# Performance work log

Measured on AMD Instinct MI355X. Metric: run time of the kernel, lower is better.

## Reference

```python
import jax, jax.numpy as jnp
import numpy as np

# bitsandbytes NF4 codebook (16 levels)
NF4_CODE = jnp.array([
    -1.0, -0.6961928009986877, -0.5250730514526367, -0.39491748809814453,
    -0.28444138169288635, -0.18477343022823334, -0.09105003625154495, 0.0,
    0.07958029955625534, 0.16093020141124725, 0.24611230194568634,
    0.33791524171829224, 0.44070982933044434, 0.5626170039176941,
    0.7229568362236023, 1.0], dtype=jnp.float32)

L, D, KV, F, V = 2, 4096, 1024, 14336, 32000   # layers, d_model, kv_dim, ffn, vocab
H, HK, HD = 32, 8, 128                          # q heads, kv heads, head dim
B, S = 2, 1024
BLK = 64                                        # NF4 quant blocksize
ROPE_THETA = 500000.0
RMS_EPS = 1e-5


def _dequant(idx, absmax, shape):
    # idx: uint8 flat codes in [0,16); absmax: fp32 per-64-element block scale
    w = NF4_CODE[idx.astype(jnp.int32)]
    return (w.reshape(-1, BLK) * absmax[:, None]).reshape(shape)


def _rmsnorm(x, w):
    return x * jax.lax.rsqrt(jnp.mean(x * x, axis=-1, keepdims=True) + RMS_EPS) * w


def _rope(x, cos, sin):
    d2 = x.shape[-1] // 2
    x1, x2 = x[..., :d2], x[..., d2:]
    return jnp.concatenate([x1 * cos - x2 * sin, x2 * cos + x1 * sin], axis=-1)


def setup_inputs() -> dict:
    key = jax.random.key(0)
    ks = iter(jax.random.split(key, 64))

    def idx(n):
        return jax.random.randint(next(ks), (n,), 0, 16).astype(jnp.uint8)

    def amax(n):
        return jax.random.uniform(next(ks), (n // BLK,), minval=0.01, maxval=0.05)

    def qw(n):
        return (jnp.stack([idx(n) for _ in range(L)]),
                jnp.stack([amax(n) for _ in range(L)]))

    inp = {}
    inp["input_ids"] = jax.random.randint(next(ks), (B, S), 0, V, dtype=jnp.int32)
    inp["attention_mask"] = jnp.ones((B, S), dtype=jnp.int32)
    inp["embed"] = jax.random.normal(next(ks), (V, D), dtype=jnp.float32) * 0.02
    inp["q_idx"], inp["q_absmax"] = qw(D * D)
    inp["k_idx"], inp["k_absmax"] = qw(KV * D)
    inp["v_idx"], inp["v_absmax"] = qw(KV * D)
    inp["o_idx"], inp["o_absmax"] = qw(D * D)
    inp["gate_idx"], inp["gate_absmax"] = qw(F * D)
    inp["up_idx"], inp["up_absmax"] = qw(F * D)
    inp["down_idx"], inp["down_absmax"] = qw(D * F)
    inp["ln1_w"] = jnp.ones((L, D), dtype=jnp.float32)
    inp["ln2_w"] = jnp.ones((L, D), dtype=jnp.float32)
    inp["final_ln_w"] = jnp.ones((D,), dtype=jnp.float32)
    return inp


def reference(input_ids, attention_mask, embed,
              q_idx, q_absmax, k_idx, k_absmax, v_idx, v_absmax,
              o_idx, o_absmax, gate_idx, gate_absmax, up_idx, up_absmax,
              down_idx, down_absmax, ln1_w, ln2_w, final_ln_w):
    b, s = input_ids.shape
    h = embed[input_ids]                                  # [B,S,D]
    pos = jnp.arange(s, dtype=jnp.float32)
    inv = 1.0 / (ROPE_THETA ** (jnp.arange(0, HD, 2, dtype=jnp.float32) / HD))
    ang = pos[:, None] * inv[None, :]                     # [S,HD/2]
    cos = jnp.cos(ang)[None, :, None, :]
    sin = jnp.sin(ang)[None, :, None, :]
    causal = jnp.tril(jnp.ones((s, s), dtype=bool))
    mask = causal[None, None] & (attention_mask[:, None, None, :] > 0)  # [B,1,S,S]
    neg = jnp.finfo(h.dtype).min

    for l in range(L):
        x = _rmsnorm(h, ln1_w[l])
        q = x @ _dequant(q_idx[l], q_absmax[l], (D, D)).T
        k = x @ _dequant(k_idx[l], k_absmax[l], (KV, D)).T
        v = x @ _dequant(v_idx[l], v_absmax[l], (KV, D)).T
        q = _rope(q.reshape(b, s, H, HD), cos, sin)
        k = _rope(k.reshape(b, s, HK, HD), cos, sin)
        v = v.reshape(b, s, HK, HD)
        k = jnp.repeat(k, H // HK, axis=2)                # GQA expand
        v = jnp.repeat(v, H // HK, axis=2)
        scores = jnp.einsum('bqhd,bkhd->bhqk', q, k) / np.float32(np.sqrt(HD))
        scores = jnp.where(mask, scores, neg)
        attn = jax.nn.softmax(scores, axis=-1)
        ctx = jnp.einsum('bhqk,bkhd->bqhd', attn, v).reshape(b, s, D)
        h = h + ctx @ _dequant(o_idx[l], o_absmax[l], (D, D)).T
        x = _rmsnorm(h, ln2_w[l])
        g = x @ _dequant(gate_idx[l], gate_absmax[l], (F, D)).T
        u = x @ _dequant(up_idx[l], up_absmax[l], (F, D)).T
        h = h + (jax.nn.silu(g) * u) @ _dequant(down_idx[l], down_absmax[l], (D, F)).T

    h = _rmsnorm(h, final_ln_w)                           # last hidden state
    m = attention_mask.astype(h.dtype)[..., None]         # masked mean pool
    pooled = (h * m).sum(axis=1) / jnp.clip(m.sum(axis=1), 1e-9)
    return pooled
```

## Files before the change

### kernel.cpp

```cpp
#include <hip/hip_runtime.h>
#include <hip/hip_fp16.h>
#include <cstdint>
#include <cstddef>

#define B_  2
#define S_  1024
#define D_  4096
#define KV_ 1024
#define F_  14336
#define H_  32
#define HK_ 8
#define HD_ 128
#define M_  2048

typedef _Float16 f16;
typedef f16   f16x8 __attribute__((ext_vector_type(8)));
typedef f16   f16x4 __attribute__((ext_vector_type(4)));
typedef float f32x4 __attribute__((ext_vector_type(4)));

#define AS1(p) ((const __attribute__((address_space(1))) void*)(p))
#define AS3(p) ((__attribute__((address_space(3))) void*)(p))

__device__ __constant__ float NF4_C[16] = {
 -1.0f, -0.6961928009986877f, -0.5250730514526367f, -0.39491748809814453f,
 -0.28444138169288635f, -0.18477343022823334f, -0.09105003625154495f, 0.0f,
 0.07958029955625534f, 0.16093020141124725f, 0.24611230194568634f,
 0.33791524171829224f, 0.44070982933044434f, 0.5626170039176941f,
 0.7229568362236023f, 1.0f };

__global__ void k_detect(const unsigned* __restrict__ p, int* __restrict__ flag){
    if (threadIdx.x == 0){
        int u8 = 0;
        for (int i = 0; i < 256; ++i) if (p[i] >= 16u) { u8 = 1; break; }
        *flag = u8;
    }
}

__global__ __launch_bounds__(256) void k_dequant(const void* __restrict__ idxBase, size_t elemOff,
        const float* __restrict__ amax, f16* __restrict__ out, const int* __restrict__ flag)
{
    __shared__ __half2 T[3856];
    int t = threadIdx.x;
    if (t < 256){
        int b0 = t & 15, b1 = t >> 4;
        T[b0 + (b1 << 8)] = __halves2half2(__float2half(NF4_C[b0]), __float2half(NF4_C[b1]));
    }
    __syncthreads();
    size_t i = ((size_t)blockIdx.x * 256 + t) * 16;
    float am = amax[i >> 6];
    __half2 am2 = __float2half2_rn(am);
    union { __half2 h2[8]; uint4 u4[2]; } R;
    if (*flag){
        uint4 u = *(const uint4*)((const uint8_t*)idxBase + elemOff + i);
        unsigned w[4] = {u.x, u.y, u.z, u.w};
        #pragma unroll
        for (int j = 0; j < 4; ++j){
            R.h2[j*2+0] = __hmul2(T[w[j] & 0xFFFFu], am2);
            R.h2[j*2+1] = __hmul2(T[w[j] >> 16],     am2);
        }
    } else {
        const int4* s4 = (const int4*)((const int*)idxBase + elemOff + i);
        #pragma unroll
        for (int j = 0; j < 4; ++j){
            int4 a = s4[j];
            R.h2[j*2+0] = __hmul2(T[a.x | (a.y << 8)], am2);
            R.h2[j*2+1] = __hmul2(T[a.z | (a.w << 8)], am2);
        }
    }
    uint4* o = (uint4*)(out + i);
    o[0] = R.u4[0]; o[1] = R.u4[1];
}

__global__ __launch_bounds__(256) void k_dequant3(const void* __restrict__ qi, const void* __restrict__ ki,
        const void* __restrict__ vi, const float* __restrict__ qa, const float* __restrict__ ka,
        const float* __restrict__ va, size_t oDD, size_t oKVD, f16* __restrict__ out,
        const int* __restrict__ flag)
{
    __shared__ __half2 T[3856];
    int t = threadIdx.x;
    if (t < 256){
        int b0 = t & 15, b1 = t >> 4;
        T[b0 + (b1 << 8)] = __halves2half2(__float2half(NF4_C[b0]), __float2half(NF4_C[b1]));
    }
    __syncthreads();
    int blk = blockIdx.x;
    const void* src; const float* am; size_t so; f16* dst;
    const size_t DDc = (size_t)D_ * D_, KVDc = (size_t)KV_ * D_;
    if (blk < 4096)      { src = qi; am = qa; so = oDD;  dst = out; }
    else if (blk < 5120) { src = ki; am = ka; so = oKVD; dst = out + DDc;        blk -= 4096; }
    else                 { src = vi; am = va; so = oKVD; dst = out + DDc + KVDc; blk -= 5120; }
    size_t i = ((size_t)blk * 256 + t) * 16;
    float amv = am[(so + i) >> 6];
    __half2 am2 = __float2half2_rn(amv);
    union { __half2 h2[8]; uint4 u4[2]; } R;
    if (*flag){
        uint4 u = *(const uint4*)((const uint8_t*)src + so + i);
        unsigned w[4] = {u.x, u.y, u.z, u.w};
        #pragma unroll
        for (int j = 0; j < 4; ++j){
            R.h2[j*2+0] = __hmul2(T[w[j] & 0xFFFFu], am2);
            R.h2[j*2+1] = __hmul2(T[w[j] >> 16],     am2);
        }
    } else {
        const int4* s4 = (const int4*)((const int*)src + so + i);
        #pragma unroll
        for (int j = 0; j < 4; ++j){
            int4 a = s4[j];
            R.h2[j*2+0] = __hmul2(T[a.x | (a.y << 8)], am2);
            R.h2[j*2+1] = __hmul2(T[a.z | (a.w << 8)], am2);
        }
    }
    uint4* o = (uint4*)(dst + i);
    o[0] = R.u4[0]; o[1] = R.u4[1];
}

__global__ __launch_bounds__(256) void k_embed(const int* __restrict__ ids,
        const float* __restrict__ E, float* __restrict__ Hh)
{
    int row = blockIdx.x, t = threadIdx.x;
    int id = ids[row];
    const float4* s4 = (const float4*)(E + (size_t)id * D_);
    float4* d4 = (float4*)(Hh + (size_t)row * D_);
    #pragma unroll
    for (int i = 0; i < 4; ++i) d4[t + 256*i] = s4[t + 256*i];
}

__global__ __launch_bounds__(256) void k_ropetab(float* __restrict__ cosT, float* __restrict__ sinT){
    int id = blockIdx.x * 256 + threadIdx.x;
    int d = id & 63, s = id >> 6;
    float inv = powf(500000.0f, -(float)d * (1.0f/64.0f));
    float ang = (float)s * inv;
    cosT[id] = cosf(ang);
    sinT[id] = sinf(ang);
}

__global__ void k_maskadd(const int* __restrict__ am, float* __restrict__ ma){
    int i = blockIdx.x * 256 + threadIdx.x;
    ma[i] = am[i] ? 0.f : -1e30f;
}

template<int F16OUT>
__global__ __launch_bounds__(256) void k_rmsnorm(const float* __restrict__ X,
        const float* __restrict__ W, void* __restrict__ outv)
{
    int row = blockIdx.x, t = threadIdx.x;
    const float4* x4 = (const float4*)(X + (size_t)row * D_);
    float4 xs[4]; float ss = 0.f;
    #pragma unroll
    for (int i = 0; i < 4; ++i){
        xs[i] = x4[t + 256*i];
        ss += xs[i].x*xs[i].x + xs[i].y*xs[i].y + xs[i].z*xs[i].z + xs[i].w*xs[i].w;
    }
    for (int m = 32; m; m >>= 1) ss += __shfl_xor(ss, m, 64);
    __shared__ float red[4];
    if ((t & 63) == 0) red[t >> 6] = ss;
    __syncthreads();
    ss = red[0] + red[1] + red[2] + red[3];
    float rs = rsqrtf(ss * (1.0f / D_) + 1e-5f);
    #pragma unroll
    for (int i = 0; i < 4; ++i){
        int c0 = (t + 256*i) * 4;
        float4 wv = *(const float4*)(W + c0);
        float o0 = xs[i].x*rs*wv.x, o1 = xs[i].y*rs*wv.y;
        float o2 = xs[i].z*rs*wv.z, o3 = xs[i].w*rs*wv.w;
        if (F16OUT){
            f16x4 ov = { (f16)o0, (f16)o1, (f16)o2, (f16)o3 };
            *(f16x4*)((f16*)outv + (size_t)row * D_ + c0) = ov;
        } else {
            float4 ov = {o0, o1, o2, o3};
            *(float4*)((float*)outv + (size_t)row * D_ + c0) = ov;
        }
    }
}

template<int F16OUT>
__global__ __launch_bounds__(256) void k_combnorm(float* __restrict__ H,
        const float* __restrict__ p0, const float* __restrict__ p1,
        const float* __restrict__ W, void* __restrict__ outv)
{
    int row = blockIdx.x, t = threadIdx.x;
    size_t base = (size_t)row * D_;
    float4 xs[4]; float ss = 0.f;
    #pragma unroll
    for (int i = 0; i < 4; ++i){
        int c4 = (t + 256*i) * 4;
        float4 hv = *(const float4*)(H + base + c4);
        float4 a  = *(const float4*)(p0 + base + c4);
        float4 b  = *(const float4*)(p1 + base + c4);
        hv.x += a.x + b.x; hv.y += a.y + b.y; hv.z += a.z + b.z; hv.w += a.w + b.w;
        *(float4*)(H + base + c4) = hv;
        xs[i] = hv;
        ss += hv.x*hv.x + hv.y*hv.y + hv.z*hv.z + hv.w*hv.w;
    }
    for (int m = 32; m; m >>= 1) ss += __shfl_xor(ss, m, 64);
    __shared__ float red[4];
    if ((t & 63) == 0) red[t >> 6] = ss;
    __syncthreads();
    ss = red[0] + red[1] + red[2] + red[3];
    float rs = rsqrtf(ss * (1.0f / D_) + 1e-5f);
    #pragma unroll
    for (int i = 0; i < 4; ++i){
        int c0 = (t + 256*i) * 4;
        float4 wv = *(const float4*)(W + c0);
        float o0 = xs[i].x*rs*wv.x, o1 = xs[i].y*rs*wv.y;
        float o2 = xs[i].z*rs*wv.z, o3 = xs[i].w*rs*wv.w;
        if (F16OUT){
            f16x4 ov = { (f16)o0, (f16)o1, (f16)o2, (f16)o3 };
            *(f16x4*)((f16*)outv + base + c0) = ov;
        } else {
            float4 ov = {o0, o1, o2, o3};
            *(float4*)((float*)outv + base + c0) = ov;
        }
    }
}

template<int LNH>
__global__ __launch_bounds__(256) void k_rope(const f16* __restrict__ in, int istr,
        f16* __restrict__ outp, const float* __restrict__ cosT, const float* __restrict__ sinT)
{
    int p = blockIdx.x * 256 + threadIdx.x;
    int d = p & 63;
    int h = (p >> 6) & ((1 << LNH) - 1);
    int s = (p >> (6 + LNH)) & (S_ - 1);
    int b = p >> (16 + LNH);
    size_t ib = (size_t)(b * S_ + s) * istr + (size_t)h * HD_;
    float x1 = (float)in[ib + d], x2 = (float)in[ib + 64 + d];
    float c = cosT[s*64 + d], sn = sinT[s*64 + d];
    size_t ob = (((size_t)((b << LNH) + h)) * S_ + (size_t)s) * HD_;
    outp[ob + d]      = (f16)(x1 * c - x2 * sn);
    outp[ob + 64 + d] = (f16)(x2 * c + x1 * sn);
}

__global__ __launch_bounds__(256) void k_vtrans(const f16* __restrict__ in, int istr,
        f16* __restrict__ outp){
    int p = blockIdx.x * 256 + threadIdx.x;
    int s  = p & (S_ - 1);
    int d  = (p >> 10) & (HD_ - 1);
    int hk = (p >> 17) & (HK_ - 1);
    int b  = p >> 20;
    f16 v = in[(size_t)(b * S_ + s) * istr + (size_t)hk * HD_ + d];
    outp[(((size_t)(b * HK_ + hk)) * HD_ + d) * S_ + s] = v;
}

__global__ __launch_bounds__(256) void k_flash(const f16* __restrict__ Qr, const f16* __restrict__ Kr,
        const f16* __restrict__ Vt, const float* __restrict__ mAddG, f16* __restrict__ ctx)
{
    __shared__ f16 KS[8192];
    __shared__ f16 VS[8192];
    __shared__ f16 PS[8192];
    const int t = threadIdx.x;
    const int w = t >> 6, l = t & 63;
    const int lr = l & 15, lg = l >> 4;
    const int qt = blockIdx.x, bh = blockIdx.y;
    const int b = bh >> 5, hh = bh & 31, hk = hh >> 2;
    const f16* Qb = Qr + ((size_t)bh * S_ + (size_t)qt*128) * HD_;
    const f16* Kb = Kr + (size_t)(b * HK_ + hk) * S_ * HD_;
    const f16* Vb = Vt + (size_t)(b * HK_ + hk) * HD_ * S_;

    auto stage16x128 = [&](const f16* src, int lds_, f16* dst){
        int rowl = t >> 4;
        int cs = ((t & 15) ^ (rowl & 7)) << 3;
        #pragma unroll
        for (int g = 0; g < 4; ++g)
            __builtin_amdgcn_global_load_lds(AS1(src + (size_t)(g*16 + rowl)*lds_ + cs),
                AS3(dst + g*2048 + w*512), 16, 0, 0);
    };
    auto stage32x64 = [&](const f16* src, int lds_, f16* dst){
        int rowl = t >> 3;
        int cs = ((t & 7) ^ (rowl & 7)) << 3;
        #pragma unroll
        for (int g = 0; g < 4; ++g)
            __builtin_amdgcn_global_load_lds(AS1(src + (size_t)(g*32 + rowl)*lds_ + cs),
                AS3(dst + g*2048 + w*512), 16, 0, 0);
    };

    stage16x128(Qb, HD_, KS);
    stage16x128(Qb + 64*HD_, HD_, VS);
    __syncthreads();
    f16x8 qF[2][4];
    {
        const f16* qsrc = (w < 2) ? KS : VS;
        int rbase = (w & 1) * 32;
        #pragma unroll
        for (int m = 0; m < 2; ++m)
            #pragma unroll
            for (int kd = 0; kd < 4; ++kd){
                int row = rbase + m*16 + lr;
                qF[m][kd] = *(const f16x8*)&qsrc[row*128 + (((kd*4 + lg) ^ (row & 7)) << 3)];
            }
    }
    __syncthreads();

    float mrow[2][4], lrow[2][4];
    f32x4 oacc[2][8];
    #pragma unroll
    for (int m = 0; m < 2; ++m)
        #pragma unroll
        for (int r = 0; r < 4; ++r){ mrow[m][r] = -1e30f; lrow[m][r] = 0.f; }
    #pragma unroll
    for (int m = 0; m < 2; ++m)
        #pragma unroll
        for (int dn = 0; dn < 8; ++dn){ f32x4 z = {0,0,0,0}; oacc[m][dn] = z; }

    const float ISQ = 0.08838834764831845f;
    const int ktMax = 2*qt + 1;

    for (int kt = 0; kt <= ktMax; ++kt){
        stage16x128(Kb + (size_t)(kt*64)*HD_, HD_, KS);
        __syncthreads();

        f32x4 sacc[2][4];
        #pragma unroll
        for (int m = 0; m < 2; ++m)
            #pragma unroll
            for (int n = 0; n < 4; ++n){ f32x4 z = {0,0,0,0}; sacc[m][n] = z; }
        #pragma unroll
        for (int n = 0; n < 4; ++n){
            int krow = n*16 + lr;
            #pragma unroll
            for (int kd = 0; kd < 4; ++kd){
                f16x8 kF = *(const f16x8*)&KS[krow*128 + (((kd*4 + lg) ^ (krow & 7)) << 3)];
                #pragma unroll
                for (int m = 0; m < 2; ++m)
                    sacc[m][n] = __builtin_amdgcn_mfma_f32_16x16x32_f16(qF[m][kd], kF, sacc[m][n], 0, 0, 0);
            }
        }

        stage32x64(Vb + kt*64, S_, VS);

        float mAdd[4];
        #pragma unroll
        for (int n = 0; n < 4; ++n) mAdd[n] = mAddG[b*S_ + kt*64 + n*16 + lr];
        int diag = (kt >= 2*qt);
        #pragma unroll
        for (int m = 0; m < 2; ++m)
        #pragma unroll
        for (int n = 0; n < 4; ++n)
        #pragma unroll
        for (int r = 0; r < 4; ++r){
            float s = sacc[m][n][r] * ISQ + mAdd[n];
            if (diag && (kt*64 + n*16 + lr) > (qt*128 + w*32 + m*16 + lg*4 + r)) s = -1e30f;
            sacc[m][n][r] = s;
        }
        #pragma unroll
        for (int m = 0; m < 2; ++m)
        #pragma unroll
        for (int r = 0; r < 4; ++r){
            float tm = fmaxf(fmaxf(sacc[m][0][r], sacc[m][1][r]), fmaxf(sacc[m][2][r], sacc[m][3][r]));
            #pragma unroll
            for (int msk = 1; msk < 16; msk <<= 1) tm = fmaxf(tm, __shfl_xor(tm, msk, 64));
            float mn = fmaxf(mrow[m][r], tm);
            float scl = __expf(mrow[m][r] - mn);
            mrow[m][r] = mn;
            float rs = 0.f;
            #pragma unroll
            for (int n = 0; n < 4; ++n){
                float p = __expf(sacc[m][n][r] - mn);
                sacc[m][n][r] = p; rs += p;
            }
            #pragma unroll
            for (int msk = 1; msk < 16; msk <<= 1) rs += __shfl_xor(rs, msk, 64);
            lrow[m][r] = lrow[m][r] * scl + rs;
            #pragma unroll
            for (int dn = 0; dn < 8; ++dn) oacc[m][dn][r] *= scl;
        }
        #pragma unroll
        for (int m = 0; m < 2; ++m)
        #pragma unroll
        for (int n = 0; n < 4; ++n)
        #pragma unroll
        for (int r = 0; r < 4; ++r){
            int rowl = m*16 + lg*4 + r;
            int slot = (n*2 + (lr >> 3)) ^ (rowl & 7);
            PS[w*2048 + rowl*64 + slot*8 + (lr & 7)] = (f16)sacc[m][n][r];
        }
        __syncthreads();

        f16x8 pF[2][2];
        #pragma unroll
        for (int m = 0; m < 2; ++m)
            #pragma unroll
            for (int kd = 0; kd < 2; ++kd){
                int prow = m*16 + lr;
                pF[m][kd] = *(const f16x8*)&PS[w*2048 + prow*64 + (((kd*4 + lg) ^ (prow & 7)) << 3)];
            }
        #pragma unroll
        for (int dn = 0; dn < 8; ++dn){
            int vrow = dn*16 + lr;
            #pragma unroll
            for (int kd = 0; kd < 2; ++kd){
                f16x8 vF = *(const f16x8*)&VS[vrow*64 + (((kd*4 + lg) ^ (vrow & 7)) << 3)];
                #pragma unroll
                for (int m = 0; m < 2; ++m)
                    oacc[m][dn] = __builtin_amdgcn_mfma_f32_16x16x32_f16(pF[m][kd], vF, oacc[m][dn], 0, 0, 0);
            }
        }
        __syncthreads();
    }

    #pragma unroll
    for (int m = 0; m < 2; ++m)
    #pragma unroll
    for (int dn = 0; dn < 8; ++dn)
    #pragma unroll
    for (int r = 0; r < 4; ++r){
        int grow = qt*128 + w*32 + m*16 + lg*4 + r;
        int gcol = hh*128 + dn*16 + lr;
        float v = oacc[m][dn][r] / fmaxf(lrow[m][r], 1e-30f);
        ctx[((size_t)(b * S_) + grow) * D_ + gcol] = (f16)v;
    }
}

template<int OUT>
__global__ __launch_bounds__(512, 1) void k_gemm3(const f16* __restrict__ A, const f16* __restrict__ Bp,
        void* __restrict__ Cv, const f16* __restrict__ G, int Kd, int ldk, int ldc)
{
    __shared__ f16 LDS[65536];
    const int t = threadIdx.x;
    const int w = t >> 6, l = t & 63;
    const int wm = w >> 2, wn = w & 3;

    int gx = gridDim.x, gy = gridDim.y;
    int nWG = gx * gy * gridDim.z;
    int n = (blockIdx.z * gy + blockIdx.y) * gx + blockIdx.x;
    int q = nWG >> 3;
    int sw = (n & 7) * q + (n >> 3);
    int by = sw % gy; int r1 = sw / gy; int bx = r1 % gx; int bz = r1 / gx;

    const int row0 = by * 256, col0 = bx * 256;
    const size_t koff = (size_t)bz * Kd;
    const int NT = Kd >> 6;

    const int swzk = ((t & 7) ^ ((t >> 3) & 7)) * 8;
    const f16* pA[2]; const f16* pB[2];
    #pragma unroll
    for (int l2 = 0; l2 < 2; ++l2){
        pA[l2] = A  + (size_t)(row0 + l2*128 + (t >> 3)) * ldk + koff + swzk;
        int wnc = (l2*64 + (t >> 3)) >> 5;
        pB[l2] = Bp + (size_t)(col0 + wnc*64 + ((t >> 3) & 31)) * ldk + koff + swzk;
    }

    auto stA = [&](int g, int tt, int buf){
        size_t so = (size_t)tt * 64;
        #pragma unroll
        for (int l2 = 0; l2 < 2; ++l2)
            __builtin_amdgcn_global_load_lds(AS1(pA[l2] + (size_t)g*64*ldk + so),
                AS3(&LDS[buf*16384 + g*8192 + l2*4096 + w*512]), 16, 0, 0);
    };
    auto stB = [&](int g, int tt, int buf){
        size_t so = (size_t)tt * 64;
        #pragma unroll
        for (int l2 = 0; l2 < 2; ++l2)
            __builtin_amdgcn_global_load_lds(AS1(pB[l2] + (size_t)g*32*ldk + so),
                AS3(&LDS[32768 + buf*16384 + g*8192 + l2*4096 + w*512]), 16, 0, 0);
    };

    const int lrow = (l & 15) * 64;
    const int kp0 = (((l >> 4))     ^ (l & 7)) * 8;
    const int kp1 = ((4 + (l >> 4)) ^ (l & 7)) * 8;

    f16x8 aR[2][4], bR0[2][2], bR1[2][2];
    auto rdA = [&](int g, int buf){
        int base = buf*16384 + g*8192 + wm*4096 + lrow;
        #pragma unroll
        for (int mf = 0; mf < 4; ++mf){
            aR[0][mf] = *(const f16x8*)&LDS[base + mf*1024 + kp0];
            aR[1][mf] = *(const f16x8*)&LDS[base + mf*1024 + kp1];
        }
    };
    auto rdB = [&](int g, int buf, f16x8 (&bR)[2][2]){
        int base = 32768 + buf*16384 + g*8192 + wn*2048 + lrow;
        #pragma unroll
        for (int nf = 0; nf < 2; ++nf){
            bR[0][nf] = *(const f16x8*)&LDS[base + nf*1024 + kp0];
            bR[1][nf] = *(const f16x8*)&LDS[base + nf*1024 + kp1];
        }
    };

    f32x4 zero = {0.f, 0.f, 0.f, 0.f};
    f32x4 acc[8][4];
    #pragma unroll
    for (int mi = 0; mi < 8; ++mi)
        #pragma unroll
        for (int ni = 0; ni < 4; ++ni) acc[mi][ni] = zero;

    #define MMQ(qm, qn, bR) { \
        __builtin_amdgcn_s_setprio(1); \
        _Pragma("unroll") \
        for (int ks = 0; ks < 2; ++ks) \
            _Pragma("unroll") \
            for (int mf = 0; mf < 4; ++mf) \
                _Pragma("unroll") \
                for (int nf = 0; nf < 2; ++nf) \
                    acc[(qm)*4+mf][(qn)*2+nf] = __builtin_amdgcn_mfma_f32_16x16x32_f16(aR[ks][mf], bR[ks][nf], acc[(qm)*4+mf][(qn)*2+nf], 0, 0, 0); \
        __builtin_amdgcn_s_setprio(0); }
    #define LGKM0 { asm volatile("s_waitcnt lgkmcnt(0)" ::: "memory"); __builtin_amdgcn_sched_barrier(0); }
    #define VM4   { asm volatile("s_waitcnt vmcnt(4)" ::: "memory"); }
    #define BAR   __builtin_amdgcn_s_barrier()

    stA(0, 0, 0); stB(1, 0, 0); stA(1, 0, 0); stB(0, 0, 0);
    if (NT > 1){ stA(0, 1, 1); stB(1, 1, 1); }
    VM4; BAR;

    for (int tt = 0; tt < NT; tt += 2){
        int c2 = (tt + 2 < NT) ? tt + 2 : NT - 1;
        int c3 = (tt + 3 < NT) ? tt + 3 : NT - 1;
        rdA(0, 0); rdB(0, 0, bR0);
        stA(1, tt+1 < NT ? tt+1 : NT-1, 1); stB(0, tt+1 < NT ? tt+1 : NT-1, 1);
        BAR; LGKM0; MMQ(0, 0, bR0); BAR;
        rdB(1, 0, bR1);
        BAR; LGKM0; MMQ(0, 1, bR1); BAR;
        rdA(1, 0);
        stA(0, c2, 0);
        BAR; LGKM0; MMQ(1, 1, bR1); BAR;
        stB(1, c2, 0);
        BAR; MMQ(1, 0, bR0); VM4; BAR;
        rdA(0, 1); rdB(0, 1, bR0);
        stA(1, c2, 0); stB(0, c2, 0);
        BAR; LGKM0; MMQ(0, 0, bR0); BAR;
        rdB(1, 1, bR1);
        BAR; LGKM0; MMQ(0, 1, bR1); BAR;
        rdA(1, 1);
        stA(0, c3, 1);
        BAR; LGKM0; MMQ(1, 1, bR1); BAR;
        stB(1, c3, 1);
        BAR; MMQ(1, 0, bR0); VM4; BAR;
    }

    #pragma unroll
    for (int mi = 0; mi < 8; ++mi)
    #pragma unroll
    for (int ni = 0; ni < 4; ++ni)
    #pragma unroll
    for (int r = 0; r < 4; ++r){
        int row = row0 + wm*128 + mi*16 + ((l >> 4) << 2) + r;
        int col = col0 + wn*64  + ni*16 + (l & 15);
        float v = acc[mi][ni][r];
        if (OUT == 0){
            ((float*)Cv)[(size_t)bz * ((size_t)M_ * ldc) + (size_t)row * ldc + col] = v;
        } else if (OUT == 2){
            ((f16*)Cv)[(size_t)row * ldc + col] = (f16)v;
        } else {
            size_t idx = (size_t)row * ldc + col;
            float g = (float)G[idx];
            float sg = g / (1.f + __expf(-g));
            ((f16*)Cv)[idx] = (f16)(sg * v);
        }
    }
    #undef MMQ
    #undef LGKM0
    #undef VM4
    #undef BAR
}

__global__ __launch_bounds__(256) void k_pool1(const float* __restrict__ Hn, const int* __restrict__ amask,
        float* __restrict__ part, float* __restrict__ cntp)
{
    int d0 = blockIdx.x * 256 + threadIdx.x;
    int b  = blockIdx.y;
    int z  = blockIdx.z;
    int s0 = z * 128;
    float s = 0.f;
    for (int i = 0; i < 128; ++i){
        int row = s0 + i;
        if (amask[b * S_ + row])
            s += Hn[((size_t)(b * S_ + row)) * D_ + d0];
    }
    part[((size_t)(z * B_ + b)) * D_ + d0] = s;
    if (blockIdx.x == 0 && threadIdx.x == 0){
        float c = 0.f;
        for (int i = 0; i < 128; ++i) c += (amask[b * S_ + s0 + i] != 0) ? 1.f : 0.f;
        cntp[z * B_ + b] = c;
    }
}
__global__ __launch_bounds__(256) void k_pool2(const float* __restrict__ part, const float* __restrict__ cntp,
        float* __restrict__ outp)
{
    int gid = blockIdx.x * 256 + threadIdx.x;
    int b = gid >> 12, d = gid & (D_ - 1);
    float s = 0.f, c = 0.f;
    #pragma unroll
    for (int z = 0; z < 8; ++z){
        s += part[((size_t)(z * B_ + b)) * D_ + d];
        c += cntp[z * B_ + b];
    }
    outp[gid] = s / fmaxf(c, 1e-9f);
}

extern "C" void kernel_launch(void* const* d_in, const int* in_sizes, int n_in,
                              void* d_out, int out_size, void* d_ws, size_t ws_size,
                              hipStream_t stream)
{
    (void)in_sizes; (void)n_in; (void)out_size; (void)ws_size;
    const int*   ids   = (const int*)  d_in[0];
    const int*   amask = (const int*)  d_in[1];
    const float* embed = (const float*)d_in[2];
    const void*  qi = d_in[3];  const float* qa = (const float*)d_in[4];
    const void*  ki = d_in[5];  const float* ka = (const float*)d_in[6];
    const void*  vi = d_in[7];  const float* va = (const float*)d_in[8];
    const void*  oi = d_in[9];  const float* oa = (const float*)d_in[10];
    const void*  gi = d_in[11]; const float* ga = (const float*)d_in[12];
    const void*  ui = d_in[13]; const float* ua = (const float*)d_in[14];
    const void*  di = d_in[15]; const float* da = (const float*)d_in[16];
    const float* ln1 = (const float*)d_in[17];
    const float* ln2 = (const float*)d_in[18];
    const float* lnf = (const float*)d_in[19];

    const size_t DD  = (size_t)D_ * D_;
    const size_t KVD = (size_t)KV_ * D_;
    const size_t FD  = (size_t)F_ * D_;

    char* ws = (char*)d_ws;
    int*   flag = (int*)ws;
    float* h    = (float*)(ws + 256);
    float* cosT = (float*)(ws + 256 + 33554432);
    float* sinT = cosT + 65536;
    f16*   xin  = (f16*)(ws + 34078976);
    f16*   wbuf = (f16*)(ws + 50856192);
    char*  R4   = ws + 168296704;
    f16* qkv16 = (f16*)(R4);
    f16* qr  = (f16*)(R4 + 25165824);
    f16* kr  = (f16*)(R4 + 41943040);
    f16* vtr = (f16*)(R4 + 46137344);
    f16* ctx = (f16*)(R4 + 50331648);
    char* R5 = R4 + 67108864;
    f16*    gbuf   = (f16*)R5;
    float*  pR5_0  = (float*)R5;
    float*  pR5_1  = (float*)(R5 + 33554432);
    float*  pR4_0  = (float*)R4;
    float*  pR4_1  = (float*)(R4 + 33554432);
    float*  hn     = (float*)R4;
    float*  part   = (float*)R5;
    float*  cntp   = (float*)(R5 + 1048576);
    float*  maskAdd= (float*)(ws + 310378496);

    const int QKV_N = D_ + 2 * KV_;

    k_detect <<<1, 64, 0, stream>>>((const unsigned*)qi, flag);
    k_embed  <<<M_, 256, 0, stream>>>(ids, embed, h);
    k_ropetab<<<256, 256, 0, stream>>>(cosT, sinT);
    k_maskadd<<<(B_*S_)/256, 256, 0, stream>>>(amask, maskAdd);
    k_rmsnorm<1><<<M_, 256, 0, stream>>>(h, ln1, xin);

    for (int l = 0; l < 2; ++l){
        size_t oDD = (size_t)l * DD, oKVD = (size_t)l * KVD, oFD = (size_t)l * FD;

        k_dequant3<<<6144, 256, 0, stream>>>(qi, ki, vi, qa, ka, va, oDD, oKVD, wbuf, flag);
        k_gemm3<2><<<dim3(QKV_N/256, M_/256, 1), 512, 0, stream>>>(xin, wbuf, qkv16, nullptr, D_, D_, QKV_N);

        k_rope<5><<<(B_*S_*H_*64)/256, 256, 0, stream>>>(qkv16, QKV_N, qr, cosT, sinT);
        k_rope<3><<<(B_*S_*HK_*64)/256, 256, 0, stream>>>(qkv16 + D_, QKV_N, kr, cosT, sinT);
        k_vtrans <<<(B_*HK_*HD_*S_)/256, 256, 0, stream>>>(qkv16 + D_ + KV_, QKV_N, vtr);

        k_flash<<<dim3(S_/128, B_*H_), 256, 0, stream>>>(qr, kr, vtr, maskAdd, ctx);

        k_dequant<<<DD / 4096, 256, 0, stream>>>(oi, oDD, oa + oDD/64, wbuf, flag);
        k_gemm3<0><<<dim3(D_/256, M_/256, 2), 512, 0, stream>>>(ctx, wbuf, pR5_0, nullptr, D_/2, D_, D_);
        k_combnorm<1><<<M_, 256, 0, stream>>>(h, pR5_0, pR5_1, ln2 + l * D_, xin);

        k_dequant<<<FD / 4096, 256, 0, stream>>>(gi, oFD, ga + oFD/64, wbuf, flag);
        k_gemm3<2><<<dim3(F_/256, M_/256, 1), 512, 0, stream>>>(xin, wbuf, gbuf, nullptr, D_, D_, F_);
        k_dequant<<<FD / 4096, 256, 0, stream>>>(ui, oFD, ua + oFD/64, wbuf, flag);
        k_gemm3<3><<<dim3(F_/256, M_/256, 1), 512, 0, stream>>>(xin, wbuf, gbuf, gbuf, D_, D_, F_);
        k_dequant<<<FD / 4096, 256, 0, stream>>>(di, oFD, da + oFD/64, wbuf, flag);
        k_gemm3<0><<<dim3(D_/256, M_/256, 2), 512, 0, stream>>>(gbuf, wbuf, pR4_0, nullptr, F_/2, F_, D_);

        if (l == 0)
            k_combnorm<1><<<M_, 256, 0, stream>>>(h, pR4_0, pR4_1, ln1 + D_, xin);
        else
            k_combnorm<0><<<M_, 256, 0, stream>>>(h, pR4_0, pR4_1, lnf, hn);
    }

    k_pool1<<<dim3(D_/256, B_, 8), 256, 0, stream>>>(hn, amask, part, cntp);
    k_pool2<<<(B_*D_)/256, 256, 0, stream>>>(part, cntp, (float*)d_out);
}
```

Baseline: 2.470 ms.

## Dequantize all layer weights in one upfront kernel and fuse rope/vtrans

All NF4 weights for both layers are dequantized in a single large launch into a dedicated fp16 weight cache. The per-matrix dequant launches inside the layer loop are removed. The separate q-rope, k-rope and V-transpose kernels are merged into one k_qkvprep launch. This cuts launch count and keeps the dequant work as one long streaming pass, at the cost of a much larger workspace of about 872MB of fp16 weights.

```diff
diff --git a/kernel.cpp b/kernel.cpp
--- a/kernel.cpp
+++ b/kernel.cpp
@@ -28,6 +28,12 @@
  0.33791524171829224f, 0.44070982933044434f, 0.5626170039176941f,
  0.7229568362236023f, 1.0f };
 
+#define WC_LAYER  218103808ull
+#define WC_O      25165824ull
+#define WC_G      41943040ull
+#define WC_U      100663296ull
+#define WC_D      159383552ull
+
 __global__ void k_detect(const unsigned* __restrict__ p, int* __restrict__ flag){
     if (threadIdx.x == 0){
         int u8 = 0;
@@ -36,8 +42,14 @@
     }
 }
 
-__global__ __launch_bounds__(256) void k_dequant(const void* __restrict__ idxBase, size_t elemOff,
-        const float* __restrict__ amax, f16* __restrict__ out, const int* __restrict__ flag)
+__global__ __launch_bounds__(256) void k_dequant_all(
+        const void* __restrict__ qi, const void* __restrict__ ki, const void* __restrict__ vi,
+        const void* __restrict__ oi, const void* __restrict__ gi, const void* __restrict__ ui,
+        const void* __restrict__ di,
+        const float* __restrict__ qa, const float* __restrict__ ka, const float* __restrict__ va,
+        const float* __restrict__ oa, const float* __restrict__ ga, const float* __restrict__ ua,
+        const float* __restrict__ da,
+        f16* __restrict__ wc, const int* __restrict__ flag)
 {
     __shared__ __half2 T[3856];
     int t = threadIdx.x;
@@ -46,49 +58,19 @@
         T[b0 + (b1 << 8)] = __halves2half2(__float2half(NF4_C[b0]), __float2half(NF4_C[b1]));
     }
     __syncthreads();
-    size_t i = ((size_t)blockIdx.x * 256 + t) * 16;
-    float am = amax[i >> 6];
-    __half2 am2 = __float2half2_rn(am);
-    union { __half2 h2[8]; uint4 u4[2]; } R;
-    if (*flag){
-        uint4 u = *(const uint4*)((const uint8_t*)idxBase + elemOff + i);
-        unsigned w[4] = {u.x, u.y, u.z, u.w};
-        #pragma unroll
-        for (int j = 0; j < 4; ++j){
-            R.h2[j*2+0] = __hmul2(T[w[j] & 0xFFFFu], am2);
-            R.h2[j*2+1] = __hmul2(T[w[j] >> 16],     am2);
-        }
-    } else {
-        const int4* s4 = (const int4*)((const int*)idxBase + elemOff + i);
-        #pragma unroll
-        for (int j = 0; j < 4; ++j){
-            int4 a = s4[j];
-            R.h2[j*2+0] = __hmul2(T[a.x | (a.y << 8)], am2);
-            R.h2[j*2+1] = __hmul2(T[a.z | (a.w << 8)], am2);
-        }
-    }
-    uint4* o = (uint4*)(out + i);
-    o[0] = R.u4[0]; o[1] = R.u4[1];
-}
-
-__global__ __launch_bounds__(256) void k_dequant3(const void* __restrict__ qi, const void* __restrict__ ki,
-        const void* __restrict__ vi, const float* __restrict__ qa, const float* __restrict__ ka,
-        const float* __restrict__ va, size_t oDD, size_t oKVD, f16* __restrict__ out,
-        const int* __restrict__ flag)
-{
-    __shared__ __half2 T[3856];
-    int t = threadIdx.x;
-    if (t < 256){
-        int b0 = t & 15, b1 = t >> 4;
-        T[b0 + (b1 << 8)] = __halves2half2(__float2half(NF4_C[b0]), __float2half(NF4_C[b1]));
-    }
-    __syncthreads();
     int blk = blockIdx.x;
+    int l = blk / 53248; blk -= l * 53248;
+    const size_t DDc = (size_t)D_ * D_, KVDc = (size_t)KV_ * D_, FDc = (size_t)F_ * D_;
+    size_t oDD = (size_t)l * DDc, oKVD = (size_t)l * KVDc, oFD = (size_t)l * FDc;
+    f16* wl = wc + (size_t)l * WC_LAYER;
     const void* src; const float* am; size_t so; f16* dst;
-    const size_t DDc = (size_t)D_ * D_, KVDc = (size_t)KV_ * D_;
-    if (blk < 4096)      { src = qi; am = qa; so = oDD;  dst = out; }
-    else if (blk < 5120) { src = ki; am = ka; so = oKVD; dst = out + DDc;        blk -= 4096; }
-    else                 { src = vi; am = va; so = oKVD; dst = out + DDc + KVDc; blk -= 5120; }
+    if (blk < 4096)       { src = qi; am = qa; so = oDD;  dst = wl; }
+    else if (blk < 5120)  { src = ki; am = ka; so = oKVD; dst = wl + DDc;        blk -= 4096; }
+    else if (blk < 6144)  { src = vi; am = va; so = oKVD; dst = wl + DDc + KVDc; blk -= 5120; }
+    else if (blk < 10240) { src = oi; am = oa; so = oDD;  dst = wl + WC_O;       blk -= 6144; }
+    else if (blk < 24576) { src = gi; am = ga; so = oFD;  dst = wl + WC_G;       blk -= 10240; }
+    else if (blk < 38912) { src = ui; am = ua; so = oFD;  dst = wl + WC_U;       blk -= 24576; }
+    else                  { src = di; am = da; so = oFD;  dst = wl + WC_D;       blk -= 38912; }
     size_t i = ((size_t)blk * 256 + t) * 16;
     float amv = am[(so + i) >> 6];
     __half2 am2 = __float2half2_rn(amv);
@@ -214,32 +196,45 @@
     }
 }
 
-template<int LNH>
-__global__ __launch_bounds__(256) void k_rope(const f16* __restrict__ in, int istr,
-        f16* __restrict__ outp, const float* __restrict__ cosT, const float* __restrict__ sinT)
-{
-    int p = blockIdx.x * 256 + threadIdx.x;
-    int d = p & 63;
-    int h = (p >> 6) & ((1 << LNH) - 1);
-    int s = (p >> (6 + LNH)) & (S_ - 1);
-    int b = p >> (16 + LNH);
-    size_t ib = (size_t)(b * S_ + s) * istr + (size_t)h * HD_;
-    float x1 = (float)in[ib + d], x2 = (float)in[ib + 64 + d];
-    float c = cosT[s*64 + d], sn = sinT[s*64 + d];
-    size_t ob = (((size_t)((b << LNH) + h)) * S_ + (size_t)s) * HD_;
-    outp[ob + d]      = (f16)(x1 * c - x2 * sn);
-    outp[ob + 64 + d] = (f16)(x2 * c + x1 * sn);
-}
-
-__global__ __launch_bounds__(256) void k_vtrans(const f16* __restrict__ in, int istr,
-        f16* __restrict__ outp){
-    int p = blockIdx.x * 256 + threadIdx.x;
-    int s  = p & (S_ - 1);
-    int d  = (p >> 10) & (HD_ - 1);
-    int hk = (p >> 17) & (HK_ - 1);
-    int b  = p >> 20;
-    f16 v = in[(size_t)(b * S_ + s) * istr + (size_t)hk * HD_ + d];
-    outp[(((size_t)(b * HK_ + hk)) * HD_ + d) * S_ + s] = v;
+__global__ __launch_bounds__(256) void k_qkvprep(const f16* __restrict__ qkv,
+        f16* __restrict__ qr, f16* __restrict__ kr, f16* __restrict__ vtr,
+        const float* __restrict__ cosT, const float* __restrict__ sinT)
+{
+    const int istr = D_ + 2 * KV_;
+    int blk = blockIdx.x;
+    if (blk < 16384){
+        int p = blk * 256 + threadIdx.x;
+        int d = p & 63;
+        int h = (p >> 6) & 31;
+        int s = (p >> 11) & (S_ - 1);
+        int b = p >> 21;
+        size_t ib = (size_t)(b * S_ + s) * istr + (size_t)h * HD_;
+        float x1 = (float)qkv[ib + d], x2 = (float)qkv[ib + 64 + d];
+        float c = cosT[s*64 + d], sn = sinT[s*64 + d];
+        size_t ob = (((size_t)((b << 5) + h)) * S_ + (size_t)s) * HD_;
+        qr[ob + d]      = (f16)(x1 * c - x2 * sn);
+        qr[ob + 64 + d] = (f16)(x2 * c + x1 * sn);
+    } else if (blk < 20480){
+        int p = (blk - 16384) * 256 + threadIdx.x;
+        int d = p & 63;
+        int h = (p >> 6) & 7;
+        int s = (p >> 9) & (S_ - 1);
+        int b = p >> 19;
+        size_t ib = (size_t)(b * S_ + s) * istr + (size_t)(D_) + (size_t)h * HD_;
+        float x1 = (float)qkv[ib + d], x2 = (float)qkv[ib + 64 + d];
+        float c = cosT[s*64 + d], sn = sinT[s*64 + d];
+        size_t ob = (((size_t)((b << 3) + h)) * S_ + (size_t)s) * HD_;
+        kr[ob + d]      = (f16)(x1 * c - x2 * sn);
+        kr[ob + 64 + d] = (f16)(x2 * c + x1 * sn);
+    } else {
+        int p = (blk - 20480) * 256 + threadIdx.x;
+        int s  = p & (S_ - 1);
+        int d  = (p >> 10) & (HD_ - 1);
+        int hk = (p >> 17) & (HK_ - 1);
+        int b  = p >> 20;
+        f16 v = qkv[(size_t)(b * S_ + s) * istr + (size_t)(D_ + KV_) + (size_t)hk * HD_ + d];
+        vtr[(((size_t)(b * HK_ + hk)) * HD_ + d) * S_ + s] = v;
+    }
 }
 
 __global__ __launch_bounds__(256) void k_flash(const f16* __restrict__ Qr, const f16* __restrict__ Kr,
@@ -606,17 +601,12 @@
     const float* ln2 = (const float*)d_in[18];
     const float* lnf = (const float*)d_in[19];
 
-    const size_t DD  = (size_t)D_ * D_;
-    const size_t KVD = (size_t)KV_ * D_;
-    const size_t FD  = (size_t)F_ * D_;
-
     char* ws = (char*)d_ws;
     int*   flag = (int*)ws;
     float* h    = (float*)(ws + 256);
     float* cosT = (float*)(ws + 256 + 33554432);
     float* sinT = cosT + 65536;
     f16*   xin  = (f16*)(ws + 34078976);
-    f16*   wbuf = (f16*)(ws + 50856192);
     char*  R4   = ws + 168296704;
     f16* qkv16 = (f16*)(R4);
     f16* qr  = (f16*)(R4 + 25165824);
@@ -633,37 +623,32 @@
     float*  part   = (float*)R5;
     float*  cntp   = (float*)(R5 + 1048576);
     float*  maskAdd= (float*)(ws + 310378496);
+    f16*    wc     = (f16*)(ws + 335544320);
 
     const int QKV_N = D_ + 2 * KV_;
 
     k_detect <<<1, 64, 0, stream>>>((const unsigned*)qi, flag);
+    k_dequant_all<<<2*53248, 256, 0, stream>>>(qi, ki, vi, oi, gi, ui, di,
+            qa, ka, va, oa, ga, ua, da, wc, flag);
     k_embed  <<<M_, 256, 0, stream>>>(ids, embed, h);
     k_ropetab<<<256, 256, 0, stream>>>(cosT, sinT);
     k_maskadd<<<(B_*S_)/256, 256, 0, stream>>>(amask, maskAdd);
     k_rmsnorm<1><<<M_, 256, 0, stream>>>(h, ln1, xin);
 
     for (int l = 0; l < 2; ++l){
-        size_t oDD = (size_t)l * DD, oKVD = (size_t)l * KVD, oFD = (size_t)l * FD;
-
-        k_dequant3<<<6144, 256, 0, stream>>>(qi, ki, vi, qa, ka, va, oDD, oKVD, wbuf, flag);
-        k_gemm3<2><<<dim3(QKV_N/256, M_/256, 1), 512, 0, stream>>>(xin, wbuf, qkv16, nullptr, D_, D_, QKV_N);
-
-        k_rope<5><<<(B_*S_*H_*64)/256, 256, 0, stream>>>(qkv16, QKV_N, qr, cosT, sinT);
-        k_rope<3><<<(B_*S_*HK_*64)/256, 256, 0, stream>>>(qkv16 + D_, QKV_N, kr, cosT, sinT);
-        k_vtrans <<<(B_*HK_*HD_*S_)/256, 256, 0, stream>>>(qkv16 + D_ + KV_, QKV_N, vtr);
+        f16* wcl = wc + (size_t)l * WC_LAYER;
+
+        k_gemm3<2><<<dim3(QKV_N/256, M_/256, 1), 512, 0, stream>>>(xin, wcl, qkv16, nullptr, D_, D_, QKV_N);
+        k_qkvprep<<<28672, 256, 0, stream>>>(qkv16, qr, kr, vtr, cosT, sinT);
 
         k_flash<<<dim3(S_/128, B_*H_), 256, 0, stream>>>(qr, kr, vtr, maskAdd, ctx);
 
-        k_dequant<<<DD / 4096, 256, 0, stream>>>(oi, oDD, oa + oDD/64, wbuf, flag);
-        k_gemm3<0><<<dim3(D_/256, M_/256, 2), 512, 0, stream>>>(ctx, wbuf, pR5_0, nullptr, D_/2, D_, D_);
+        k_gemm3<0><<<dim3(D_/256, M_/256, 2), 512, 0, stream>>>(ctx, wcl + WC_O, pR5_0, nullptr, D_/2, D_, D_);
         k_combnorm<1><<<M_, 256, 0, stream>>>(h, pR5_0, pR5_1, ln2 + l * D_, xin);
 
-        k_dequant<<<FD / 4096, 256, 0, stream>>>(gi, oFD, ga + oFD/64, wbuf, flag);
-        k_gemm3<2><<<dim3(F_/256, M_/256, 1), 512, 0, stream>>>(xin, wbuf, gbuf, nullptr, D_, D_, F_);
-        k_dequant<<<FD / 4096, 256, 0, stream>>>(ui, oFD, ua + oFD/64, wbuf, flag);
-        k_gemm3<3><<<dim3(F_/256, M_/256, 1), 512, 0, stream>>>(xin, wbuf, gbuf, gbuf, D_, D_, F_);
-        k_dequant<<<FD / 4096, 256, 0, stream>>>(di, oFD, da + oFD/64, wbuf, flag);
-        k_gemm3<0><<<dim3(D_/256, M_/256, 2), 512, 0, stream>>>(gbuf, wbuf, pR4_0, nullptr, F_/2, F_, D_);
+        k_gemm3<2><<<dim3(F_/256, M_/256, 1), 512, 0, stream>>>(xin, wcl + WC_G, gbuf, nullptr, D_, D_, F_);
+        k_gemm3<3><<<dim3(F_/256, M_/256, 1), 512, 0, stream>>>(xin, wcl + WC_U, gbuf, gbuf, D_, D_, F_);
+        k_gemm3<0><<<dim3(D_/256, M_/256, 2), 512, 0, stream>>>(gbuf, wcl + WC_D, pR4_0, nullptr, F_/2, F_, D_);
 
         if (l == 0)
             k_combnorm<1><<<M_, 256, 0, stream>>>(h, pR4_0, pR4_1, ln1 + D_, xin);
```

After: 2.452 ms. Within noise of the previous version (-0.7%).
